# Optimization experiments

Hardware: AMD Instinct MI355X
Metric: run time of the kernel (lower is better)

Reference implementation:

```python
import math
import jax, jax.numpy as jnp
import numpy as np

N, M, DK, DV = 4096, 4096, 512, 512

def setup_inputs() -> dict:
    key = jax.random.key(0)
    k1, k2, k3, k4, k5 = jax.random.split(key, 5)
    return {
        "query": jax.random.normal(k1, (1, N, DK), dtype=jnp.float32),
        "q_k":   jax.random.normal(k2, (1, N, DK), dtype=jnp.float32),
        "q_v":   jax.random.normal(k3, (1, N, DV), dtype=jnp.float32),
        "key":   jax.random.normal(k4, (1, M, DK), dtype=jnp.float32),
        "value": jax.random.normal(k5, (1, M, DV), dtype=jnp.float32),
    }

def reference(query, q_k, q_v, key, value):
    dk = query.shape[-1]
    # diagonal of query[0] @ q_k[0].T without materializing the NxN product
    q_att = jnp.einsum('nd,nd->n', query[0], q_k[0])[:, None]      # [N, 1]
    scores = query[0] @ key[0].T                                    # [N, M]
    scores = jnp.concatenate([scores, q_att], axis=-1)[None]        # [1, N, M+1]
    scores = scores / math.sqrt(dk + 1)
    attention = jax.nn.softmax(scores, axis=-1)                     # [1, N, M+1]
    res = attention[:, :, :-1] @ value                              # [1, N, DV]
    return q_v * q_att + res
```

## Files before the change

### kernel.cpp

```cpp
#include <hip/hip_runtime.h>

#define NQ 4096
#define MK 4096
#define DKC 512
#define DVC 512
#define SCALE 0.044151079f

typedef __attribute__((ext_vector_type(8))) short short8;
typedef __attribute__((ext_vector_type(4))) float f32x4;

__device__ __forceinline__ unsigned short f2bf(float x) {
  unsigned u = __float_as_uint(x);
  u += 0x7fffu + ((u >> 16) & 1u);
  return (unsigned short)(u >> 16);
}
__device__ __forceinline__ float bf2f(unsigned short h) {
  return __uint_as_float((unsigned)h << 16);
}

#define GLL16(g, l)                                                        \
  __builtin_amdgcn_global_load_lds(                                        \
      (const __attribute__((address_space(1))) unsigned int*)(g),          \
      (__attribute__((address_space(3))) unsigned int*)(l), 16, 0, 0)

__global__ __launch_bounds__(256) void prep_all(const float* __restrict__ query,
                                                const float* __restrict__ q_k,
                                                const float* __restrict__ key,
                                                const float* __restrict__ value,
                                                unsigned short* __restrict__ Qb,
                                                unsigned short* __restrict__ Kb,
                                                unsigned short* __restrict__ Vt,
                                                float* __restrict__ qatt) {
  int b = blockIdx.x;
  if (b < 1024) {
    int n = b * 4 + (threadIdx.x >> 6);
    int lane = threadIdx.x & 63;
    const float4* qr = (const float4*)(query + (size_t)n * DKC + lane * 8);
    const float4* kr = (const float4*)(q_k + (size_t)n * DKC + lane * 8);
    float4 a0 = qr[0], a1 = qr[1];
    float4 b0 = kr[0], b1 = kr[1];
    float dot = a0.x * b0.x + a0.y * b0.y + a0.z * b0.z + a0.w * b0.w +
                a1.x * b1.x + a1.y * b1.y + a1.z * b1.z + a1.w * b1.w;
    unsigned short h[8] = {f2bf(a0.x * SCALE), f2bf(a0.y * SCALE), f2bf(a0.z * SCALE),
                           f2bf(a0.w * SCALE), f2bf(a1.x * SCALE), f2bf(a1.y * SCALE),
                           f2bf(a1.z * SCALE), f2bf(a1.w * SCALE)};
    *(short8*)(Qb + (size_t)n * DKC + lane * 8) = *(short8*)h;
#pragma unroll
    for (int off = 1; off < 64; off <<= 1) dot += __shfl_xor(dot, off, 64);
    if (lane == 0) qatt[n] = dot;
  } else if (b < 2048) {
    int i = (b - 1024) * 256 + threadIdx.x;
    const float4* src = (const float4*)key + (size_t)i * 2;
    float4 a0 = src[0], a1 = src[1];
    unsigned short h[8] = {f2bf(a0.x), f2bf(a0.y), f2bf(a0.z), f2bf(a0.w),
                           f2bf(a1.x), f2bf(a1.y), f2bf(a1.z), f2bf(a1.w)};
    *(short8*)(Kb + (size_t)i * 8) = *(short8*)h;
  } else {
    __shared__ float t[32][33];
    int bi = b - 2048;
    int tx = threadIdx.x & 31, ty = threadIdx.x >> 5;
    int m0 = (bi & 127) * 32;
    int d0 = (bi >> 7) * 32;
#pragma unroll
    for (int i = 0; i < 4; ++i)
      t[ty + i * 8][tx] = value[(size_t)(m0 + ty + i * 8) * DVC + d0 + tx];
    __syncthreads();
#pragma unroll
    for (int i = 0; i < 4; ++i)
      Vt[(size_t)(d0 + ty + i * 8) * MK + m0 + tx] = f2bf(t[tx][ty + i * 8]);
  }
}

__global__ __launch_bounds__(256, 4) void gemm_s(const unsigned short* __restrict__ Qb,
                                                 const unsigned short* __restrict__ Kb,
                                                 unsigned short* __restrict__ S,
                                                 float* __restrict__ rowsum_part) {
  __shared__ __align__(16) char lds[33792];
  const int tid = threadIdx.x;
  const int wid = tid >> 6, lane = tid & 63, lr = lane & 15, lh = lane >> 4;
  const int wm = wid >> 1, wn = wid & 1;

  int bid = blockIdx.x;
  int swz = (bid & 7) * 128 + (bid >> 3);
  const int tm = swz >> 5, tn = swz & 31;
  const size_t m0 = (size_t)tm * 128, n0 = (size_t)tn * 128;

  f32x4 acc[4][4];
#pragma unroll
  for (int i = 0; i < 4; ++i)
#pragma unroll
    for (int j = 0; j < 4; ++j) acc[i][j] = (f32x4){0.f, 0.f, 0.f, 0.f};

  const char* abase = (const char*)Qb + m0 * 1024;
  const char* bbase = (const char*)Kb + n0 * 1024;

  for (int ks = 0; ks < 8; ++ks) {
    const int kb = ks * 128;
    {
      char* al = lds;
      char* bl = lds + 16384;
#pragma unroll
      for (int s = 0; s < 4; ++s) {
        int obase = wid * 4096 + s * 1024;
        int o = obase + lane * 16;
        int row = o >> 7;
        int colg = ((o >> 4) & 7) ^ (row & 7);
        GLL16(abase + (size_t)row * 1024 + kb + colg * 16, al + obase);
        GLL16(bbase + (size_t)row * 1024 + kb + colg * 16, bl + obase);
      }
    }
    __syncthreads();
#pragma unroll
    for (int kk = 0; kk < 2; ++kk) {
      short8 af[4], bf[4];
#pragma unroll
      for (int i = 0; i < 4; ++i) {
        int ar = wm * 64 + i * 16 + lr;
        af[i] = *(const short8*)(lds + ar * 128 + ((((kk << 2) + lh) ^ (lr & 7)) << 4));
        int br = wn * 64 + i * 16 + lr;
        bf[i] = *(const short8*)(lds + 16384 + br * 128 + ((((kk << 2) + lh) ^ (lr & 7)) << 4));
      }
#pragma unroll
      for (int i = 0; i < 4; ++i)
#pragma unroll
        for (int j = 0; j < 4; ++j)
          acc[i][j] = __builtin_amdgcn_mfma_f32_16x16x32_bf16(af[i], bf[j], acc[i][j], 0, 0, 0);
    }
    __syncthreads();
  }

  unsigned short* sl = (unsigned short*)lds;
  float* rs = (float*)(lds + 32768);
  float rsum[4][4];
#pragma unroll
  for (int i = 0; i < 4; ++i)
#pragma unroll
    for (int r = 0; r < 4; ++r) rsum[i][r] = 0.f;
#pragma unroll
  for (int i = 0; i < 4; ++i)
#pragma unroll
    for (int j = 0; j < 4; ++j)
#pragma unroll
      for (int r = 0; r < 4; ++r) {
        int m = wm * 64 + i * 16 + lh * 4 + r;
        int n = wn * 64 + j * 16 + lr;
        float e = __expf(acc[i][j][r]);
        sl[m * 128 + n] = f2bf(e);
        rsum[i][r] += e;
      }
#pragma unroll
  for (int i = 0; i < 4; ++i)
#pragma unroll
    for (int r = 0; r < 4; ++r) {
      float v = rsum[i][r];
      v += __shfl_xor(v, 1, 64);
      v += __shfl_xor(v, 2, 64);
      v += __shfl_xor(v, 4, 64);
      v += __shfl_xor(v, 8, 64);
      if (lr == 0) rs[wn * 128 + wm * 64 + i * 16 + lh * 4 + r] = v;
    }
  __syncthreads();
  if (tid < 128) rowsum_part[(size_t)tn * NQ + m0 + tid] = rs[tid] + rs[128 + tid];
#pragma unroll
  for (int i = 0; i < 8; ++i) {
    int o = i * 4096 + tid * 16;
    int row = o >> 8, colb = o & 255;
    *(uint4*)((char*)S + (m0 + row) * 8192 + n0 * 2 + colb) = *(const uint4*)((const char*)sl + o);
  }
}

__global__ __launch_bounds__(512, 1) void gemm_o_part(const unsigned short* __restrict__ P,
                                                      const unsigned short* __restrict__ Vt,
                                                      unsigned short* __restrict__ part) {
  __shared__ __align__(16) char lds[98304];
  const int tid = threadIdx.x;
  const int wid = tid >> 6, lane = tid & 63, lr = lane & 15, lh = lane >> 4;
  const int wm = wid >> 2, wn = wid & 3;

  int bid = blockIdx.x;
  int swz = (bid & 7) * 32 + (bid >> 3);
  const int ksl = swz & 3;
  const int nt = (swz >> 2) & 1;
  const int mt = swz >> 3;
  const size_t m0 = (size_t)mt * 128, n0 = (size_t)nt * 256;

  f32x4 acc[4][4];
#pragma unroll
  for (int i = 0; i < 4; ++i)
#pragma unroll
    for (int j = 0; j < 4; ++j) acc[i][j] = (f32x4){0.f, 0.f, 0.f, 0.f};

  const char* abase = (const char*)P + m0 * 8192 + (size_t)ksl * 2048;
  const char* bbase = (const char*)Vt + n0 * 8192 + (size_t)ksl * 2048;

  auto stage = [&](int ks, int b) {
    const int kb = ks * 128;
    char* al = lds + b * 49152;
    char* bl = al + 16384;
#pragma unroll
    for (int s = 0; s < 2; ++s) {
      int obase = wid * 2048 + s * 1024;
      int o = obase + lane * 16;
      int row = o >> 7;
      int colg = ((o >> 4) & 7) ^ (row & 7);
      GLL16(abase + (size_t)row * 8192 + kb + colg * 16, al + obase);
    }
#pragma unroll
    for (int s = 0; s < 4; ++s) {
      int obase = wid * 4096 + s * 1024;
      int o = obase + lane * 16;
      int row = o >> 7;
      int colg = ((o >> 4) & 7) ^ (row & 7);
      GLL16(bbase + (size_t)row * 8192 + kb + colg * 16, bl + obase);
    }
  };

  stage(0, 0);

  for (int ks = 0; ks < 16; ++ks) {
    const int cur = ks & 1;
    if (ks + 1 < 16) {
      stage(ks + 1, cur ^ 1);
      asm volatile("s_waitcnt vmcnt(6)" ::: "memory");
    } else {
      asm volatile("s_waitcnt vmcnt(0)" ::: "memory");
    }
    __builtin_amdgcn_s_barrier();
    asm volatile("" ::: "memory");

    const char* al = lds + cur * 49152;
    const char* bl = al + 16384;
#pragma unroll
    for (int kk = 0; kk < 2; ++kk) {
      short8 af[4], bf[4];
#pragma unroll
      for (int i = 0; i < 4; ++i) {
        int ar = wm * 64 + i * 16 + lr;
        af[i] = *(const short8*)(al + ar * 128 + ((((kk << 2) + lh) ^ (lr & 7)) << 4));
        int br = wn * 64 + i * 16 + lr;
        bf[i] = *(const short8*)(bl + br * 128 + ((((kk << 2) + lh) ^ (lr & 7)) << 4));
      }
#pragma unroll
      for (int i = 0; i < 4; ++i)
#pragma unroll
        for (int j = 0; j < 4; ++j)
          acc[i][j] = __builtin_amdgcn_mfma_f32_16x16x32_bf16(af[i], bf[j], acc[i][j], 0, 0, 0);
    }

    asm volatile("" ::: "memory");
    __builtin_amdgcn_s_barrier();
    asm volatile("" ::: "memory");
  }

  unsigned short* sl = (unsigned short*)lds;
#pragma unroll
  for (int i = 0; i < 4; ++i)
#pragma unroll
    for (int j = 0; j < 4; ++j)
#pragma unroll
      for (int r = 0; r < 4; ++r) {
        int m = wm * 64 + i * 16 + lh * 4 + r;
        int n = wn * 64 + j * 16 + lr;
        sl[m * 256 + n] = f2bf(acc[i][j][r]);
      }
  __builtin_amdgcn_s_barrier();
  asm volatile("" ::: "memory");
  char* pbase = (char*)part + (size_t)ksl * NQ * DVC * 2;
#pragma unroll
  for (int i = 0; i < 8; ++i) {
    int o = i * 8192 + tid * 16;
    int row = o >> 9, colb = o & 511;
    *(uint4*)(pbase + (m0 + row) * 1024 + n0 * 2 + colb) = *(const uint4*)((const char*)sl + o);
  }
}

__global__ __launch_bounds__(256) void row_inv(const float* __restrict__ rowsum_part,
                                               const float* __restrict__ qatt,
                                               float* __restrict__ inv) {
  int n = blockIdx.x * 256 + threadIdx.x;
  float s = 0.f;
#pragma unroll
  for (int tn = 0; tn < 32; ++tn) s += rowsum_part[(size_t)tn * NQ + n];
  inv[n] = 1.0f / (s + __expf(qatt[n] * SCALE));
}

__global__ __launch_bounds__(256) void combine2(const unsigned short* __restrict__ part,
                                                const float* __restrict__ qatt,
                                                const float* __restrict__ inv,
                                                const float* __restrict__ q_v,
                                                float* __restrict__ out) {
  int idx = blockIdx.x * blockDim.x + threadIdx.x;
  int n = idx >> 6;
  int d8 = (idx & 63) * 8;
  float qa = qatt[n];
  float iv = inv[n];
  size_t off = (size_t)n * DVC + d8;
  float r[8] = {0.f, 0.f, 0.f, 0.f, 0.f, 0.f, 0.f, 0.f};
#pragma unroll
  for (int w = 0; w < 4; ++w) {
    short8 po = *(const short8*)(part + (size_t)w * NQ * DVC + off);
#pragma unroll
    for (int j = 0; j < 8; ++j) r[j] += bf2f((unsigned short)po[j]);
  }
  const float4* qv = (const float4*)(q_v + off);
  float4 qv0 = qv[0], qv1 = qv[1];
  float4 o0 = {qv0.x * qa + r[0] * iv, qv0.y * qa + r[1] * iv, qv0.z * qa + r[2] * iv,
               qv0.w * qa + r[3] * iv};
  float4 o1 = {qv1.x * qa + r[4] * iv, qv1.y * qa + r[5] * iv, qv1.z * qa + r[6] * iv,
               qv1.w * qa + r[7] * iv};
  float4* op = (float4*)(out + off);
  op[0] = o0;
  op[1] = o1;
}

extern "C" void kernel_launch(void* const* d_in, const int* in_sizes, int n_in,
                              void* d_out, int out_size, void* d_ws, size_t ws_size,
                              hipStream_t stream) {
  const float* query = (const float*)d_in[0];
  const float* q_k = (const float*)d_in[1];
  const float* q_v = (const float*)d_in[2];
  const float* key = (const float*)d_in[3];
  const float* value = (const float*)d_in[4];
  float* out = (float*)d_out;

  char* ws = (char*)d_ws;
  unsigned short* Qb = (unsigned short*)(ws);
  unsigned short* Kb = (unsigned short*)(ws + (4u << 20));
  unsigned short* Vt = (unsigned short*)(ws + (8u << 20));
  unsigned short* S = (unsigned short*)(ws + (12u << 20));
  float* qatt = (float*)(ws + (44u << 20));
  unsigned short* part = (unsigned short*)(ws + (45u << 20));
  float* rowsum_part = (float*)(ws + (61u << 20));
  float* inv = (float*)(ws + (62u << 20));

  prep_all<<<dim3(4096), dim3(256), 0, stream>>>(query, q_k, key, value, Qb, Kb, Vt, qatt);
  gemm_s<<<dim3(1024), dim3(256), 0, stream>>>(Qb, Kb, S, rowsum_part);
  gemm_o_part<<<dim3(256), dim3(512), 0, stream>>>(S, Vt, part);
  row_inv<<<dim3(16), dim3(256), 0, stream>>>(rowsum_part, qatt, inv);
  combine2<<<dim3(1024), dim3(256), 0, stream>>>(part, qatt, inv, q_v, out);
}
```

Before: 68.16 us.

## Shrink gemm_o_part tiles to 128x128 with single-buffered LDS for higher occupancy

Changes the second GEMM from 512-thread blocks with 128x256 tiles and double-buffered 96KB LDS to 256-thread blocks with 128x128 tiles, a single 32KB LDS buffer, and twice as many blocks. The goal is to fill all CUs and let several blocks share a CU, so cross-block concurrency hides load latency instead of explicit prefetch. In exchange, within-block overlap of global loads and MFMA is lost, and the narrower tiles re-read the P operand more often.

```diff
diff --git a/kernel.cpp b/kernel.cpp
--- a/kernel.cpp
+++ b/kernel.cpp
@@ -169,20 +169,20 @@
   }
 }
 
-__global__ __launch_bounds__(512, 1) void gemm_o_part(const unsigned short* __restrict__ P,
+__global__ __launch_bounds__(256, 4) void gemm_o_part(const unsigned short* __restrict__ P,
                                                       const unsigned short* __restrict__ Vt,
                                                       unsigned short* __restrict__ part) {
-  __shared__ __align__(16) char lds[98304];
+  __shared__ __align__(16) char lds[32768];
   const int tid = threadIdx.x;
   const int wid = tid >> 6, lane = tid & 63, lr = lane & 15, lh = lane >> 4;
-  const int wm = wid >> 2, wn = wid & 3;
+  const int wm = wid >> 1, wn = wid & 1;
 
   int bid = blockIdx.x;
-  int swz = (bid & 7) * 32 + (bid >> 3);
+  int swz = (bid & 7) * 64 + (bid >> 3);
+  const int mt = swz >> 4;
+  const int nt = (swz >> 2) & 3;
   const int ksl = swz & 3;
-  const int nt = (swz >> 2) & 1;
-  const int mt = swz >> 3;
-  const size_t m0 = (size_t)mt * 128, n0 = (size_t)nt * 256;
+  const size_t m0 = (size_t)mt * 128, n0 = (size_t)nt * 128;
 
   f32x4 acc[4][4];
 #pragma unroll
@@ -193,52 +193,31 @@
   const char* abase = (const char*)P + m0 * 8192 + (size_t)ksl * 2048;
   const char* bbase = (const char*)Vt + n0 * 8192 + (size_t)ksl * 2048;
 
-  auto stage = [&](int ks, int b) {
+  for (int ks = 0; ks < 16; ++ks) {
     const int kb = ks * 128;
-    char* al = lds + b * 49152;
-    char* bl = al + 16384;
-#pragma unroll
-    for (int s = 0; s < 2; ++s) {
-      int obase = wid * 2048 + s * 1024;
-      int o = obase + lane * 16;
-      int row = o >> 7;
-      int colg = ((o >> 4) & 7) ^ (row & 7);
-      GLL16(abase + (size_t)row * 8192 + kb + colg * 16, al + obase);
-    }
-#pragma unroll
-    for (int s = 0; s < 4; ++s) {
-      int obase = wid * 4096 + s * 1024;
-      int o = obase + lane * 16;
-      int row = o >> 7;
-      int colg = ((o >> 4) & 7) ^ (row & 7);
-      GLL16(bbase + (size_t)row * 8192 + kb + colg * 16, bl + obase);
-    }
-  };
-
-  stage(0, 0);
-
-  for (int ks = 0; ks < 16; ++ks) {
-    const int cur = ks & 1;
-    if (ks + 1 < 16) {
-      stage(ks + 1, cur ^ 1);
-      asm volatile("s_waitcnt vmcnt(6)" ::: "memory");
-    } else {
-      asm volatile("s_waitcnt vmcnt(0)" ::: "memory");
-    }
-    __builtin_amdgcn_s_barrier();
-    asm volatile("" ::: "memory");
-
-    const char* al = lds + cur * 49152;
-    const char* bl = al + 16384;
+    {
+      char* al = lds;
+      char* bl = lds + 16384;
+#pragma unroll
+      for (int s = 0; s < 4; ++s) {
+        int obase = wid * 4096 + s * 1024;
+        int o = obase + lane * 16;
+        int row = o >> 7;
+        int colg = ((o >> 4) & 7) ^ (row & 7);
+        GLL16(abase + (size_t)row * 8192 + kb + colg * 16, al + obase);
+        GLL16(bbase + (size_t)row * 8192 + kb + colg * 16, bl + obase);
+      }
+    }
+    __syncthreads();
 #pragma unroll
     for (int kk = 0; kk < 2; ++kk) {
       short8 af[4], bf[4];
 #pragma unroll
       for (int i = 0; i < 4; ++i) {
         int ar = wm * 64 + i * 16 + lr;
-        af[i] = *(const short8*)(al + ar * 128 + ((((kk << 2) + lh) ^ (lr & 7)) << 4));
+        af[i] = *(const short8*)(lds + ar * 128 + ((((kk << 2) + lh) ^ (lr & 7)) << 4));
         int br = wn * 64 + i * 16 + lr;
-        bf[i] = *(const short8*)(bl + br * 128 + ((((kk << 2) + lh) ^ (lr & 7)) << 4));
+        bf[i] = *(const short8*)(lds + 16384 + br * 128 + ((((kk << 2) + lh) ^ (lr & 7)) << 4));
       }
 #pragma unroll
       for (int i = 0; i < 4; ++i)
@@ -246,10 +225,7 @@
         for (int j = 0; j < 4; ++j)
           acc[i][j] = __builtin_amdgcn_mfma_f32_16x16x32_bf16(af[i], bf[j], acc[i][j], 0, 0, 0);
     }
-
-    asm volatile("" ::: "memory");
-    __builtin_amdgcn_s_barrier();
-    asm volatile("" ::: "memory");
+    __syncthreads();
   }
 
   unsigned short* sl = (unsigned short*)lds;
@@ -261,15 +237,14 @@
       for (int r = 0; r < 4; ++r) {
         int m = wm * 64 + i * 16 + lh * 4 + r;
         int n = wn * 64 + j * 16 + lr;
-        sl[m * 256 + n] = f2bf(acc[i][j][r]);
-      }
-  __builtin_amdgcn_s_barrier();
-  asm volatile("" ::: "memory");
+        sl[m * 128 + n] = f2bf(acc[i][j][r]);
+      }
+  __syncthreads();
   char* pbase = (char*)part + (size_t)ksl * NQ * DVC * 2;
 #pragma unroll
   for (int i = 0; i < 8; ++i) {
-    int o = i * 8192 + tid * 16;
-    int row = o >> 9, colb = o & 511;
+    int o = i * 4096 + tid * 16;
+    int row = o >> 8, colb = o & 255;
     *(uint4*)(pbase + (m0 + row) * 1024 + n0 * 2 + colb) = *(const uint4*)((const char*)sl + o);
   }
 }
@@ -335,7 +310,7 @@
 
   prep_all<<<dim3(4096), dim3(256), 0, stream>>>(query, q_k, key, value, Qb, Kb, Vt, qatt);
   gemm_s<<<dim3(1024), dim3(256), 0, stream>>>(Qb, Kb, S, rowsum_part);
-  gemm_o_part<<<dim3(256), dim3(512), 0, stream>>>(S, Vt, part);
+  gemm_o_part<<<dim3(512), dim3(256), 0, stream>>>(S, Vt, part);
   row_inv<<<dim3(16), dim3(256), 0, stream>>>(rowsum_part, qatt, inv);
   combine2<<<dim3(1024), dim3(256), 0, stream>>>(part, qatt, inv, q_v, out);
 }
```

Result: no change. 68.94 us (+1.1%).
